# Kernel optimization log

Hardware: AMD Instinct MI355X
Metric: run time of the kernel (lower is better)

The kernel has to match this reference:

```python
import jax, jax.numpy as jnp
import numpy as np

N_NODES = 100000
N_EDGES = 1600000
IN_DIM = 128
OUT_DIM = 64
SLOPE = 0.2


def setup_inputs() -> dict:
    key = jax.random.key(0)
    k1, k2, k3, k4 = jax.random.split(key, 4)
    h = jax.random.normal(k1, (N_NODES, IN_DIM), dtype=jnp.float32)
    W = jax.random.normal(k2, (OUT_DIM, IN_DIM), dtype=jnp.float32) * (1.0 / np.sqrt(IN_DIM))
    src = jax.random.randint(k3, (N_EDGES,), 0, N_NODES, dtype=jnp.int64)
    dst = jax.random.randint(k4, (N_EDGES,), 0, N_NODES, dtype=jnp.int64)
    return {"h": h, "W": W, "src": src, "dst": dst}


def reference(h, W, src, dst):
    n = h.shape[0]
    z = h @ W.T                                   # [N, out_dim]
    z_src = z[src]                                # [E, out_dim]
    z_dst = z[dst]                                # [E, out_dim]
    e = jax.nn.leaky_relu(jnp.sum(z_src * z_dst, axis=1), negative_slope=SLOPE)  # [E]
    # segment softmax over incoming edges of each destination node
    m = jax.ops.segment_max(e, dst, num_segments=n)        # [N], -inf for isolated nodes
    ex = jnp.exp(e - m[dst])                                # [E]
    denom = jax.ops.segment_sum(ex, dst, num_segments=n)    # [N]
    alpha = ex / denom[dst]                                 # [E]
    agg = jax.ops.segment_sum(alpha[:, None] * z_src, dst, num_segments=n)  # [N, out_dim]
    return jax.nn.elu(agg)
```

## Files before the change

kernel.cpp:

```cpp
#include <hip/hip_runtime.h>
#include <math.h>

#define SLOPE 0.2f
#define LOG2E 1.4426950408889634f

__global__ __launch_bounds__(256, 8) void gemm_hist_kernel(const float* __restrict__ h,
                                                           const float* __restrict__ W,
                                                           float* __restrict__ z,
                                                           const int* __restrict__ dst,
                                                           int* __restrict__ cnt,
                                                           int* __restrict__ rank,
                                                           int n, int ne) {
    int ei = blockIdx.x * 256 + threadIdx.x;
    int base = ei * 2;
    if (base + 1 < ne) {
        int2 d = *(const int2*)(dst + base);
        int2 r;
        r.x = atomicAdd(&cnt[d.x], 1);
        r.y = atomicAdd(&cnt[d.y], 1);
        *(int2*)(rank + base) = r;
    } else if (base < ne) {
        rank[base] = atomicAdd(&cnt[dst[base]], 1);
    }

    __shared__ float ws[128][36];
    int t = threadIdx.x;
    int nblk = blockIdx.x >> 1;
    int ch0  = (blockIdx.x & 1) << 5;
    const float4* __restrict__ W4 = reinterpret_cast<const float4*>(W);
#pragma unroll
    for (int j = 0; j < 4; j++) {
        int idx = t + j * 256;
        int o  = idx >> 5;
        int kq = idx & 31;
        float4 w = W4[(size_t)(ch0 + o) * 32 + kq];
        int k = kq << 2;
        int col = o ^ ((kq & 7) << 2);
        ws[k + 0][col] = w.x; ws[k + 1][col] = w.y;
        ws[k + 2][col] = w.z; ws[k + 3][col] = w.w;
    }
    __syncthreads();

    int ng = t >> 3, og = t & 7;
    int n0 = nblk * 64 + ng * 2;
    if (n0 >= n) return;
    const float* __restrict__ hp = h + (size_t)n0 * 128;

    float acc[2][4] = {};
#pragma unroll 4
    for (int k = 0; k < 128; k += 4) {
        int m = (k >> 2) & 7;
        int colb = (og ^ m) << 2;
        float4 hv[2], wv[4];
#pragma unroll
        for (int i = 0; i < 2; i++) hv[i] = *(const float4*)(hp + i * 128 + k);
#pragma unroll
        for (int kk = 0; kk < 4; kk++) wv[kk] = *(const float4*)&ws[k + kk][colb];
#pragma unroll
        for (int i = 0; i < 2; i++) {
            acc[i][0] += hv[i].x * wv[0].x + hv[i].y * wv[1].x + hv[i].z * wv[2].x + hv[i].w * wv[3].x;
            acc[i][1] += hv[i].x * wv[0].y + hv[i].y * wv[1].y + hv[i].z * wv[2].y + hv[i].w * wv[3].y;
            acc[i][2] += hv[i].x * wv[0].z + hv[i].y * wv[1].z + hv[i].z * wv[2].z + hv[i].w * wv[3].z;
            acc[i][3] += hv[i].x * wv[0].w + hv[i].y * wv[1].w + hv[i].z * wv[2].w + hv[i].w * wv[3].w;
        }
    }
#pragma unroll
    for (int i = 0; i < 2; i++) {
        *(float4*)&z[(size_t)(n0 + i) * 64 + ch0 + og * 4] =
            make_float4(acc[i][0], acc[i][1], acc[i][2], acc[i][3]);
    }
}

__global__ __launch_bounds__(256) void scan1(const int* __restrict__ cnt,
                                             int* __restrict__ starts,
                                             int* __restrict__ bsums, int n) {
    __shared__ int ls[256];
    int tbase = blockIdx.x * 4096 + threadIdx.x * 16;
    int v[16];
    int s = 0;
#pragma unroll
    for (int k = 0; k < 16; k++) {
        int idx = tbase + k;
        int c = idx < n ? cnt[idx] : 0;
        v[k] = c; s += c;
    }
    ls[threadIdx.x] = s;
    __syncthreads();
    for (int off = 1; off < 256; off <<= 1) {
        int t = threadIdx.x >= off ? ls[threadIdx.x - off] : 0;
        __syncthreads();
        ls[threadIdx.x] += t;
        __syncthreads();
    }
    int run = ls[threadIdx.x] - s;
    if (threadIdx.x == 255) bsums[blockIdx.x] = ls[255];
#pragma unroll
    for (int k = 0; k < 16; k++) {
        int idx = tbase + k;
        if (idx < n) starts[idx] = run;
        run += v[k];
    }
}

__global__ void scan2(int* __restrict__ bsums, int nb, int* __restrict__ starts,
                      int n, int ne) {
    if (threadIdx.x == 0) {
        int run = 0;
        for (int b = 0; b < nb; b++) { int t = bsums[b]; bsums[b] = run; run += t; }
        starts[n] = ne;
    }
}

__global__ __launch_bounds__(256) void scan3(int* __restrict__ starts,
                                             const int* __restrict__ bsums, int n) {
    int i = blockIdx.x * 256 + threadIdx.x;
    if (i < n) starts[i] += bsums[i >> 12];
}

__global__ __launch_bounds__(256) void scatter8_kernel(const int* __restrict__ src,
                                                       const int* __restrict__ dst,
                                                       const int* __restrict__ starts,
                                                       const int* __restrict__ rank,
                                                       int* __restrict__ csr_src, int ne) {
    int i = blockIdx.x * 256 + threadIdx.x;
    int base = i * 8;
    if (base + 7 < ne) {
        int4 s0 = *(const int4*)(src + base),  s1 = *(const int4*)(src + base + 4);
        int4 d0 = *(const int4*)(dst + base),  d1 = *(const int4*)(dst + base + 4);
        int4 r0 = *(const int4*)(rank + base), r1 = *(const int4*)(rank + base + 4);
        csr_src[starts[d0.x] + r0.x] = s0.x;
        csr_src[starts[d0.y] + r0.y] = s0.y;
        csr_src[starts[d0.z] + r0.z] = s0.z;
        csr_src[starts[d0.w] + r0.w] = s0.w;
        csr_src[starts[d1.x] + r1.x] = s1.x;
        csr_src[starts[d1.y] + r1.y] = s1.y;
        csr_src[starts[d1.z] + r1.z] = s1.z;
        csr_src[starts[d1.w] + r1.w] = s1.w;
    } else {
        for (int r = base; r < ne; r++)
            csr_src[starts[dst[r]] + rank[r]] = src[r];
    }
}

__global__ __launch_bounds__(256) void fused_node(const float4* __restrict__ z4,
                                                  const int* __restrict__ starts,
                                                  const int* __restrict__ csr_src,
                                                  float4* __restrict__ out4, int n) {
    int node = blockIdx.x * 4 + (threadIdx.x >> 6);
    if (node >= n) return;
    int lane = threadIdx.x & 63;
    int g = lane >> 4;
    int q = lane & 15;
    int rs = starts[node], re = starts[node + 1];
    float4 zd = z4[(size_t)node * 16 + q];

    float m2 = -1e30f, denom = 0.f;
    float4 acc = make_float4(0.f, 0.f, 0.f, 0.f);

    for (int c = rs; c < re; c += 64) {
        int j = c + lane;
        int sv = j < re ? csr_src[j] : 0;
        int cn = min(64, re - c);
        bool val0 = g < cn;
        int  s0 = __shfl(sv, val0 ? g : 0);
        float4 v0 = z4[(size_t)s0 * 16 + q];
        bool val1 = 4 + g < cn;
        int  s1 = __shfl(sv, val1 ? 4 + g : 0);
        float4 v1 = z4[(size_t)s1 * 16 + q];
        for (int k = 0; k < cn; k += 4) {
            int idx2 = k + 8 + g;
            bool val2 = idx2 < cn;
            int  s2 = __shfl(sv, val2 ? idx2 : 0);
            float4 v2 = z4[(size_t)s2 * 16 + q];
            float p = v0.x * zd.x + v0.y * zd.y + v0.z * zd.z + v0.w * zd.w;
#pragma unroll
            for (int msk = 1; msk < 16; msk <<= 1) p += __shfl_xor(p, msk);
            float e = p > 0.f ? p : SLOPE * p;
            float e2 = e * LOG2E;
            e2 = val0 ? e2 : -2e30f;
            if (__any(e2 > m2)) {
                float mnew = fmaxf(m2, e2);
                float sc = exp2f(m2 - mnew);
                float ex = exp2f(e2 - mnew);
                denom = fmaf(denom, sc, ex);
                acc.x = fmaf(acc.x, sc, ex * v0.x);
                acc.y = fmaf(acc.y, sc, ex * v0.y);
                acc.z = fmaf(acc.z, sc, ex * v0.z);
                acc.w = fmaf(acc.w, sc, ex * v0.w);
                m2 = mnew;
            } else {
                float ex = exp2f(e2 - m2);
                denom += ex;
                acc.x = fmaf(ex, v0.x, acc.x);
                acc.y = fmaf(ex, v0.y, acc.y);
                acc.z = fmaf(ex, v0.z, acc.z);
                acc.w = fmaf(ex, v0.w, acc.w);
            }
            v0 = v1; val0 = val1;
            v1 = v2; val1 = val2;
        }
    }
#pragma unroll
    for (int msk = 16; msk < 64; msk <<= 1) {
        float mo  = __shfl_xor(m2, msk);
        float dno = __shfl_xor(denom, msk);
        float ax = __shfl_xor(acc.x, msk);
        float ay = __shfl_xor(acc.y, msk);
        float az = __shfl_xor(acc.z, msk);
        float aw = __shfl_xor(acc.w, msk);
        float mnew = fmaxf(m2, mo);
        float ss = exp2f(m2 - mnew), so = exp2f(mo - mnew);
        denom = fmaf(denom, ss, dno * so);
        acc.x = fmaf(acc.x, ss, ax * so);
        acc.y = fmaf(acc.y, ss, ay * so);
        acc.z = fmaf(acc.z, ss, az * so);
        acc.w = fmaf(acc.w, ss, aw * so);
        m2 = mnew;
    }
    if (lane < 16) {
        float inv = denom > 0.f ? 1.f / denom : 0.f;
        float4 r; float x;
        x = acc.x * inv; r.x = x > 0.f ? x : __expf(x) - 1.f;
        x = acc.y * inv; r.y = x > 0.f ? x : __expf(x) - 1.f;
        x = acc.z * inv; r.z = x > 0.f ? x : __expf(x) - 1.f;
        x = acc.w * inv; r.w = x > 0.f ? x : __expf(x) - 1.f;
        out4[(size_t)node * 16 + q] = r;
    }
}

extern "C" void kernel_launch(void* const* d_in, const int* in_sizes, int n_in,
                              void* d_out, int out_size, void* d_ws, size_t ws_size,
                              hipStream_t stream) {
    const float* h   = (const float*)d_in[0];
    const float* W   = (const float*)d_in[1];
    const int*   src = (const int*)d_in[2];
    const int*   dst = (const int*)d_in[3];
    int n  = in_sizes[0] / 128;
    int ne = in_sizes[2];

    float* z       = (float*)d_ws;
    int*   rank    = (int*)(z + (size_t)n * 64);
    int*   csr_src = rank + ne;
    int*   cnt     = csr_src + ne;
    int*   starts  = cnt + n;
    int*   bsums   = starts + ((n + 5) & ~3);

    int nb_gemm = ((n + 63) / 64) * 2;
    int nb_scan = (n + 4095) / 4096;

    hipMemsetAsync(cnt, 0, (size_t)n * sizeof(int), stream);
    gemm_hist_kernel<<<nb_gemm, 256, 0, stream>>>(h, W, z, dst, cnt, rank, n, ne);
    scan1<<<nb_scan, 256, 0, stream>>>(cnt, starts, bsums, n);
    scan2<<<1, 64, 0, stream>>>(bsums, nb_scan, starts, n, ne);
    scan3<<<(n + 255) / 256, 256, 0, stream>>>(starts, bsums, n);
    scatter8_kernel<<<(ne / 8 + 255) / 256, 256, 0, stream>>>(src, dst, starts,
                                                              rank, csr_src, ne);
    fused_node<<<(n + 3) / 4, 256, 0, stream>>>((const float4*)z, starts, csr_src,
                                                (float4*)d_out, n);
}
```

Before: 203.9 us.

## Split histogram into dedicated blocks and fold block-sum scan into scan3

The dst histogram atomics move out of the GEMM blocks into extra dedicated blocks of the same launch, with each thread handling four edges through an int4 load. The single-thread scan2 kernel is removed. Each scan3 block now sums the preceding scan1 block totals itself, which saves one launch and a serial pass. The cost is redundant serial reads of bsums in every scan3 block, though there are only about 25 entries. GEMM blocks no longer carry atomic latency, but the histogram blocks may compete with the GEMM blocks for occupancy.

```diff
diff --git a/kernel.cpp b/kernel.cpp
--- a/kernel.cpp
+++ b/kernel.cpp
@@ -10,17 +10,22 @@
                                                            const int* __restrict__ dst,
                                                            int* __restrict__ cnt,
                                                            int* __restrict__ rank,
-                                                           int n, int ne) {
-    int ei = blockIdx.x * 256 + threadIdx.x;
-    int base = ei * 2;
-    if (base + 1 < ne) {
-        int2 d = *(const int2*)(dst + base);
-        int2 r;
-        r.x = atomicAdd(&cnt[d.x], 1);
-        r.y = atomicAdd(&cnt[d.y], 1);
-        *(int2*)(rank + base) = r;
-    } else if (base < ne) {
-        rank[base] = atomicAdd(&cnt[dst[base]], 1);
+                                                           int n, int ne, int nbGemm) {
+    if ((int)blockIdx.x >= nbGemm) {
+        int i = (blockIdx.x - nbGemm) * 256 + threadIdx.x;
+        int base = i * 4;
+        if (base + 3 < ne) {
+            int4 d = *(const int4*)(dst + base);
+            int4 r;
+            r.x = atomicAdd(&cnt[d.x], 1);
+            r.y = atomicAdd(&cnt[d.y], 1);
+            r.z = atomicAdd(&cnt[d.z], 1);
+            r.w = atomicAdd(&cnt[d.w], 1);
+            *(int4*)(rank + base) = r;
+        } else if (base < ne) {
+            for (int rr = base; rr < ne; rr++) rank[rr] = atomicAdd(&cnt[dst[rr]], 1);
+        }
+        return;
     }
 
     __shared__ float ws[128][36];
@@ -102,19 +107,20 @@
     }
 }
 
-__global__ void scan2(int* __restrict__ bsums, int nb, int* __restrict__ starts,
-                      int n, int ne) {
+__global__ __launch_bounds__(256) void scan3(int* __restrict__ starts,
+                                             const int* __restrict__ bsums,
+                                             int n, int ne) {
+    __shared__ int base_s;
+    int i = blockIdx.x * 256 + threadIdx.x;
     if (threadIdx.x == 0) {
-        int run = 0;
-        for (int b = 0; b < nb; b++) { int t = bsums[b]; bsums[b] = run; run += t; }
-        starts[n] = ne;
-    }
-}
-
-__global__ __launch_bounds__(256) void scan3(int* __restrict__ starts,
-                                             const int* __restrict__ bsums, int n) {
-    int i = blockIdx.x * 256 + threadIdx.x;
-    if (i < n) starts[i] += bsums[i >> 12];
+        int reg = (int)(blockIdx.x >> 4);
+        int s = 0;
+        for (int b = 0; b < reg; b++) s += bsums[b];
+        base_s = s;
+        if (blockIdx.x == 0) starts[n] = ne;
+    }
+    __syncthreads();
+    if (i < n) starts[i] += base_s;
 }
 
 __global__ __launch_bounds__(256) void scatter8_kernel(const int* __restrict__ src,
@@ -245,14 +251,15 @@
     int*   starts  = cnt + n;
     int*   bsums   = starts + ((n + 5) & ~3);
 
-    int nb_gemm = ((n + 63) / 64) * 2;
+    int nbGemm = ((n + 63) / 64) * 2;
+    int nbHist = (ne / 4 + 255) / 256;
     int nb_scan = (n + 4095) / 4096;
 
     hipMemsetAsync(cnt, 0, (size_t)n * sizeof(int), stream);
-    gemm_hist_kernel<<<nb_gemm, 256, 0, stream>>>(h, W, z, dst, cnt, rank, n, ne);
+    gemm_hist_kernel<<<nbGemm + nbHist, 256, 0, stream>>>(h, W, z, dst, cnt, rank,
+                                                          n, ne, nbGemm);
     scan1<<<nb_scan, 256, 0, stream>>>(cnt, starts, bsums, n);
-    scan2<<<1, 64, 0, stream>>>(bsums, nb_scan, starts, n, ne);
-    scan3<<<(n + 255) / 256, 256, 0, stream>>>(starts, bsums, n);
+    scan3<<<(n + 255) / 256, 256, 0, stream>>>(starts, bsums, n, ne);
     scatter8_kernel<<<(ne / 8 + 255) / 256, 256, 0, stream>>>(src, dst, starts,
                                                               rank, csr_src, ne);
     fused_node<<<(n + 3) / 4, 256, 0, stream>>>((const float4*)z, starts, csr_src,
```

Result: no change. 207.0 us (+1.5%).
